# Optimization experiments

Hardware: AMD Instinct MI355X
Metric: run time of the kernel (lower is better)

The kernel has to match this reference:

```python
import jax, jax.numpy as jnp
import numpy as np

B, N, D, P = 4, 512, 512, 128

def setup_inputs() -> dict:
    key = jax.random.key(0)
    ks = jax.random.split(key, 8)
    s = lambda fan_in: 1.0 / np.sqrt(fan_in)
    inp = {
        "input": jax.random.normal(ks[0], (B, N, D), dtype=jnp.float32),
        # bigram projections (weights stored [in, out]; torch Linear is [out, in])
        "Wl": jax.random.uniform(ks[1], (D, P), jnp.float32, -s(D), s(D)),
        "bl": jnp.zeros((P,), jnp.float32),  # zeroed in initialize_parameters
        "Wr": jax.random.uniform(ks[2], (D, P), jnp.float32, -s(D), s(D)),  # no bias
        "Wo": jax.random.uniform(ks[3], (P, 1), jnp.float32, -s(P), s(P)),
        "bo": jnp.zeros((1,), jnp.float32),
        # start builder MLP
        "Ws1": jax.random.uniform(ks[4], (D, P), jnp.float32, -s(D), s(D)),
        "bs1": jnp.zeros((P,), jnp.float32),
        "Ws2": jax.random.uniform(ks[5], (P, 1), jnp.float32, -s(P), s(P)),
        "bs2": jnp.zeros((1,), jnp.float32),
        # end builder MLP
        "We1": jax.random.uniform(ks[6], (D, P), jnp.float32, -s(D), s(D)),
        "be1": jnp.zeros((P,), jnp.float32),
        "We2": jax.random.uniform(ks[7], (P, 1), jnp.float32, -s(P), s(P)),
        "be2": jnp.zeros((1,), jnp.float32),
    }
    return inp


def reference(input, Wl, bl, Wr, Wo, bo, Ws1, bs1, Ws2, bs2, We1, be1, We2, be2):
    # start / end unigram scores: [B, N, 1]
    start = jnp.maximum(input @ Ws1 + bs1, 0.0) @ Ws2 + bs2
    end = jnp.maximum(input @ We1 + be1, 0.0) @ We2 + be2
    # bigram scores
    left = input @ Wl + bl   # [B, N, P]
    right = input @ Wr       # [B, N, P]
    # left.unsqueeze(1) + right.unsqueeze(2) -> [B, N, N, P]
    proj = left[:, None, :, :] + right[:, :, None, :]
    bigram = jnp.maximum(proj, 0.0) @ Wo + bo  # [B, N, N, 1]
    return (bigram, start, end)
```

## Files before the change

kernel.cpp:

```cpp
#include <hip/hip_runtime.h>

typedef unsigned short ushort_t;
using f32x4  = __attribute__((ext_vector_type(4))) float;
using bf16x8 = __attribute__((ext_vector_type(8))) short;
using u16x8  = __attribute__((ext_vector_type(8))) unsigned short;
using h2v    = __attribute__((ext_vector_type(2))) _Float16;

constexpr int Bc = 4;
constexpr int Nc = 512;
constexpr int Dc = 512;
constexpr int Pc = 128;
constexpr int ROWS = Bc * Nc;

__device__ inline unsigned short f2bf(float f) {
    unsigned u = __builtin_bit_cast(unsigned, f);
    unsigned r = u + 0x7fffu + ((u >> 16) & 1u);
    return (unsigned short)(r >> 16);
}

__device__ inline void gload_lds16(const void* g, void* l) {
    __builtin_amdgcn_global_load_lds(
        (const __attribute__((address_space(1))) unsigned int*)g,
        (__attribute__((address_space(3))) unsigned int*)l, 16, 0, 0);
}

__device__ inline unsigned packh2(float a, float b) {
    unsigned short lo = __builtin_bit_cast(unsigned short, (_Float16)a);
    unsigned short hi = __builtin_bit_cast(unsigned short, (_Float16)b);
    return (unsigned)lo | ((unsigned)hi << 16);
}

__global__ __launch_bounds__(256) void convert_kernel(
    const float* __restrict__ input,
    const float* __restrict__ Wl,  const float* __restrict__ Wr,
    const float* __restrict__ Ws1, const float* __restrict__ We1,
    ushort_t* __restrict__ inBF2, ushort_t* __restrict__ WcatT2)
{
    const int bx = blockIdx.x, t = threadIdx.x;
    __shared__ float T[64][68];

    if (bx < 256) {
        const int mt = bx >> 3, ks = bx & 7;
        const int c = t & 7, r0 = t >> 3;
        const float* src = input + (size_t)(mt * 64) * Dc + ks * 64;
        ushort_t* dstc = inBF2 + ((size_t)(mt * 8 + ks) * 8 + c) * 512;
        #pragma unroll
        for (int h = 0; h < 2; ++h) {
            const int r = r0 + h * 32;
            const float* s = src + (size_t)r * Dc + c * 8;
            float4 v0 = *(const float4*)s;
            float4 v1 = *(const float4*)(s + 4);
            u16x8 o;
            o[0] = f2bf(v0.x); o[1] = f2bf(v0.y); o[2] = f2bf(v0.z); o[3] = f2bf(v0.w);
            o[4] = f2bf(v1.x); o[5] = f2bf(v1.y); o[6] = f2bf(v1.z); o[7] = f2bf(v1.w);
            *(u16x8*)(dstc + r * 8) = o;
        }
    } else {
        const int idx = bx - 256;
        const int nt = idx >> 3, ks = idx & 7;
        const int mi = nt >> 1, cm0 = (nt & 1) * 64;
        const float* Wm = (mi == 0) ? Wl : (mi == 1) ? Wr : (mi == 2) ? Ws1 : We1;

        const int kk_ = t >> 4, cc = (t & 15) << 2;
        #pragma unroll
        for (int u = 0; u < 4; ++u)
            *(float4*)&T[kk_ + 16 * u][cc] =
                *(const float4*)&Wm[(size_t)(ks * 64 + kk_ + 16 * u) * Pc + cm0 + cc];
        __syncthreads();

        const int col = t & 63, c2 = t >> 6;
        #pragma unroll
        for (int h = 0; h < 2; ++h) {
            const int kc = c2 + h * 4;
            u16x8 o;
            #pragma unroll
            for (int i = 0; i < 8; ++i) o[i] = f2bf(T[kc * 8 + i][col]);
            *(u16x8*)(WcatT2 + ((size_t)(nt * 8 + ks) * 8 + kc) * 512 + col * 8) = o;
        }
    }
}

__global__ __launch_bounds__(256) void mfma_proj3(
    const ushort_t* __restrict__ inBF2, const ushort_t* __restrict__ WcatT2,
    const float* __restrict__ bl,
    const float* __restrict__ bs1, const float* __restrict__ Ws2,
    const float* __restrict__ be1, const float* __restrict__ We2,
    ushort_t* __restrict__ leftH, ushort_t* __restrict__ rightH,
    float* __restrict__ parts)
{
    const int mt2 = blockIdx.x, ny = blockIdx.y;
    const int row0 = mt2 * 32;
    const int t = threadIdx.x, w = t >> 6, l = t & 63;
    const int wm = w & 1, wn = w >> 1;
    const int fr = l & 15, fg = l >> 4;

    __shared__ ushort_t As[2][2048];
    __shared__ ushort_t Bs[2][4096];
    __shared__ float red[64];

    const ushort_t* Atile = inBF2 + (size_t)(mt2 >> 1) * 8 * 4096;
    const int h32 = (mt2 & 1) * 32;
    const ushort_t* Bbase = WcatT2 + (size_t)ny * 8 * 4096;

    f32x4 acc0 = {0.f, 0.f, 0.f, 0.f}, acc1 = {0.f, 0.f, 0.f, 0.f};

#define PSTAGE(BI, KS)                                                         \
    {                                                                          \
        const ushort_t* ga = Atile + (KS) * 4096;                              \
        const ushort_t* gb = Bbase + (KS) * 4096;                              \
        gload_lds16(ga + (2 * w + (l >> 5)) * 512 + (h32 + (l & 31)) * 8,      \
                    &As[BI][w * 512]);                                         \
        gload_lds16(gb + w * 512 + l * 8, &Bs[BI][w * 512]);                   \
        gload_lds16(gb + (w + 4) * 512 + l * 8, &Bs[BI][(w + 4) * 512]);       \
    }

    PSTAGE(0, 0);
    __syncthreads();

    for (int ks = 0; ks < 8; ++ks) {
        const int bi = ks & 1;
        if (ks < 7) PSTAGE(bi ^ 1, ks + 1);
        #pragma unroll
        for (int kk = 0; kk < 2; ++kk) {
            const int kc = kk * 4 + fg;
            bf16x8 a  = *(const bf16x8*)&As[bi][kc * 256 + (wm * 16 + fr) * 8];
            bf16x8 b0 = *(const bf16x8*)&Bs[bi][kc * 512 + (wn * 32 + fr) * 8];
            bf16x8 b1 = *(const bf16x8*)&Bs[bi][kc * 512 + (wn * 32 + 16 + fr) * 8];
            acc0 = __builtin_amdgcn_mfma_f32_16x16x32_bf16(a, b0, acc0, 0, 0, 0);
            acc1 = __builtin_amdgcn_mfma_f32_16x16x32_bf16(a, b1, acc1, 0, 0, 0);
        }
        __syncthreads();
    }
#undef PSTAGE

    const int fq4 = fg << 2;
    if (ny < 4) {
        ushort_t* outp = (ny < 2) ? leftH : rightH;
        const int cb = (ny & 1) * 64 + wn * 32;
        #pragma unroll
        for (int n = 0; n < 2; ++n) {
            const int col = cb + n * 16 + fr;
            const float bv = (ny < 2) ? bl[col] : 0.f;
            const f32x4 av = n ? acc1 : acc0;
            #pragma unroll
            for (int q = 0; q < 4; ++q) {
                float v = av[q] + bv;
                outp[(size_t)(row0 + wm * 16 + fq4 + q) * Pc + col] =
                    __builtin_bit_cast(ushort_t, (_Float16)v);
            }
        }
    } else {
        const int pi = ny - 4;
        const float* b1 = (ny < 6) ? bs1 : be1;
        const float* W2 = (ny < 6) ? Ws2 : We2;
        const int pb = (pi & 1) * 64;
        #pragma unroll
        for (int q = 0; q < 4; ++q) {
            const int cp0 = pb + wn * 32 + fr;
            const int cp1 = pb + wn * 32 + 16 + fr;
            float v = fmaxf(acc0[q] + b1[cp0], 0.f) * W2[cp0]
                    + fmaxf(acc1[q] + b1[cp1], 0.f) * W2[cp1];
            v += __shfl_xor(v, 1);
            v += __shfl_xor(v, 2);
            v += __shfl_xor(v, 4);
            v += __shfl_xor(v, 8);
            if (fr == 0) red[wn * 32 + wm * 16 + fq4 + q] = v;
        }
        __syncthreads();
        if (t < 32) parts[pi * ROWS + row0 + t] = red[t] + red[32 + t];
    }
}

__global__ __launch_bounds__(256) void bigram_kernel(
    const ushort_t* __restrict__ leftH, const ushort_t* __restrict__ rightH,
    const float* __restrict__ Wo,   const float* __restrict__ bo,
    const float* __restrict__ parts,
    const float* __restrict__ bs2,  const float* __restrict__ be2,
    float* __restrict__ out, float* __restrict__ start_out,
    float* __restrict__ end_out)
{
    const int jt = blockIdx.x, it = blockIdx.y, b = blockIdx.z;
    const int t  = threadIdx.x;

    if (jt == 16) {
        const int base = (b * 8 + it) * 64;
        if (t < 64) {
            const int r = base + t;
            start_out[r] = parts[r] + parts[ROWS + r] + bs2[0];
        } else if (t < 128) {
            const int r = base + t - 64;
            end_out[r] = parts[2 * ROWS + r] + parts[3 * ROWS + r] + be2[0];
        }
        return;
    }

    __shared__ unsigned Lh[32][68];
    __shared__ unsigned Rh[64][68];
    __shared__ unsigned woh[64];

    const ushort_t* lp = leftH  + (size_t)(b * Nc + jt * 32) * Pc;
    const ushort_t* rp = rightH + (size_t)(b * Nc + it * 64) * Pc;

    #pragma unroll
    for (int u = 0; u < 2; ++u) {
        int f = t + u * 256, r = f >> 4, c = f & 15;
        *(float4*)&Lh[r][c * 4] = *(const float4*)(lp + (size_t)r * Pc + c * 8);
    }
    #pragma unroll
    for (int u = 0; u < 4; ++u) {
        int f = t + u * 256, r = f >> 4, c = f & 15;
        *(float4*)&Rh[r][c * 4] = *(const float4*)(rp + (size_t)r * Pc + c * 8);
    }
    if (t < 64) woh[t] = packh2(Wo[2 * t], Wo[2 * t + 1]);
    __syncthreads();

    const int jl = t & 15;
    const int il = t >> 4;

    float acc[4][2] = {};
    const h2v hz = {(_Float16)0.f, (_Float16)0.f};

#define DOTH(COMP)                                                       \
    {                                                                    \
        const unsigned wu = w4.COMP;                                     \
        h2v lv[2], rv[4];                                                \
        lv[0] = __builtin_bit_cast(h2v, l4[0].COMP);                     \
        lv[1] = __builtin_bit_cast(h2v, l4[1].COMP);                     \
        rv[0] = __builtin_bit_cast(h2v, r4[0].COMP);                     \
        rv[1] = __builtin_bit_cast(h2v, r4[1].COMP);                     \
        rv[2] = __builtin_bit_cast(h2v, r4[2].COMP);                     \
        rv[3] = __builtin_bit_cast(h2v, r4[3].COMP);                     \
        _Pragma("unroll") for (int ii = 0; ii < 4; ++ii)                 \
        _Pragma("unroll") for (int jj = 0; jj < 2; ++jj) {               \
            h2v sum = lv[jj] + rv[ii];                                   \
            sum = __builtin_elementwise_max(sum, hz);                    \
            unsigned su = __builtin_bit_cast(unsigned, sum);             \
            asm("v_dot2_f32_f16 %0, %1, %2, %0"                          \
                : "+v"(acc[ii][jj]) : "v"(su), "v"(wu));                 \
        }                                                                \
    }

    #pragma unroll 4
    for (int s4 = 0; s4 < 16; ++s4) {
        uint4 w4 = *(const uint4*)&woh[4 * s4];
        uint4 l4[2], r4[4];
        #pragma unroll
        for (int jj = 0; jj < 2; ++jj) l4[jj] = *(const uint4*)&Lh[jl + 16 * jj][4 * s4];
        #pragma unroll
        for (int ii = 0; ii < 4; ++ii) r4[ii] = *(const uint4*)&Rh[il + 16 * ii][4 * s4];
        DOTH(x) DOTH(y) DOTH(z) DOTH(w)
    }
#undef DOTH

    const float bias = bo[0];
    #pragma unroll
    for (int ii = 0; ii < 4; ++ii) {
        #pragma unroll
        for (int jj = 0; jj < 2; ++jj) {
            const int gi = it * 64 + il + 16 * ii;
            const int gj = jt * 32 + jl + 16 * jj;
            out[((size_t)b * Nc + gi) * Nc + gj] = acc[ii][jj] + bias;
        }
    }
}

extern "C" void kernel_launch(void* const* d_in, const int* in_sizes, int n_in,
                              void* d_out, int out_size, void* d_ws, size_t ws_size,
                              hipStream_t stream) {
    const float* input = (const float*)d_in[0];
    const float* Wl  = (const float*)d_in[1];
    const float* bl  = (const float*)d_in[2];
    const float* Wr  = (const float*)d_in[3];
    const float* Wo  = (const float*)d_in[4];
    const float* bo  = (const float*)d_in[5];
    const float* Ws1 = (const float*)d_in[6];
    const float* bs1 = (const float*)d_in[7];
    const float* Ws2 = (const float*)d_in[8];
    const float* bs2 = (const float*)d_in[9];
    const float* We1 = (const float*)d_in[10];
    const float* be1 = (const float*)d_in[11];
    const float* We2 = (const float*)d_in[12];
    const float* be2 = (const float*)d_in[13];

    float* out    = (float*)d_out;
    float* bigram = out;
    float* start  = out + (size_t)Bc * Nc * Nc;
    float* end    = start + (size_t)Bc * Nc;

    ushort_t* leftH  = (ushort_t*)d_ws;
    ushort_t* rightH = leftH + (size_t)ROWS * Pc;
    float* parts     = (float*)(rightH + (size_t)ROWS * Pc);
    ushort_t* inBF2  = (ushort_t*)(parts + 4 * ROWS);
    ushort_t* WcatT2 = inBF2 + (size_t)ROWS * Dc;

    convert_kernel<<<320, 256, 0, stream>>>(input, Wl, Wr, Ws1, We1, inBF2, WcatT2);

    mfma_proj3<<<dim3(64, 8), 256, 0, stream>>>(
        inBF2, WcatT2, bl, bs1, Ws2, be1, We2, leftH, rightH, parts);

    bigram_kernel<<<dim3(17, 8, 4), 256, 0, stream>>>(
        leftH, rightH, Wo, bo, parts, bs2, be2, bigram, start, end);
}
```

Before: 31.43 us.

## Fuse input bf16 conversion into projection GEMM A-tile loading

```diff
diff --git a/kernel.cpp b/kernel.cpp
--- a/kernel.cpp
+++ b/kernel.cpp
@@ -30,58 +30,38 @@
     return (unsigned)lo | ((unsigned)hi << 16);
 }
 
-__global__ __launch_bounds__(256) void convert_kernel(
-    const float* __restrict__ input,
+__global__ __launch_bounds__(256) void wconv_kernel(
     const float* __restrict__ Wl,  const float* __restrict__ Wr,
     const float* __restrict__ Ws1, const float* __restrict__ We1,
-    ushort_t* __restrict__ inBF2, ushort_t* __restrict__ WcatT2)
+    ushort_t* __restrict__ WcatT2)
 {
     const int bx = blockIdx.x, t = threadIdx.x;
     __shared__ float T[64][68];
 
-    if (bx < 256) {
-        const int mt = bx >> 3, ks = bx & 7;
-        const int c = t & 7, r0 = t >> 3;
-        const float* src = input + (size_t)(mt * 64) * Dc + ks * 64;
-        ushort_t* dstc = inBF2 + ((size_t)(mt * 8 + ks) * 8 + c) * 512;
-        #pragma unroll
-        for (int h = 0; h < 2; ++h) {
-            const int r = r0 + h * 32;
-            const float* s = src + (size_t)r * Dc + c * 8;
-            float4 v0 = *(const float4*)s;
-            float4 v1 = *(const float4*)(s + 4);
-            u16x8 o;
-            o[0] = f2bf(v0.x); o[1] = f2bf(v0.y); o[2] = f2bf(v0.z); o[3] = f2bf(v0.w);
-            o[4] = f2bf(v1.x); o[5] = f2bf(v1.y); o[6] = f2bf(v1.z); o[7] = f2bf(v1.w);
-            *(u16x8*)(dstc + r * 8) = o;
-        }
-    } else {
-        const int idx = bx - 256;
-        const int nt = idx >> 3, ks = idx & 7;
-        const int mi = nt >> 1, cm0 = (nt & 1) * 64;
-        const float* Wm = (mi == 0) ? Wl : (mi == 1) ? Wr : (mi == 2) ? Ws1 : We1;
-
-        const int kk_ = t >> 4, cc = (t & 15) << 2;
-        #pragma unroll
-        for (int u = 0; u < 4; ++u)
-            *(float4*)&T[kk_ + 16 * u][cc] =
-                *(const float4*)&Wm[(size_t)(ks * 64 + kk_ + 16 * u) * Pc + cm0 + cc];
-        __syncthreads();
-
-        const int col = t & 63, c2 = t >> 6;
-        #pragma unroll
-        for (int h = 0; h < 2; ++h) {
-            const int kc = c2 + h * 4;
-            u16x8 o;
-            #pragma unroll
-            for (int i = 0; i < 8; ++i) o[i] = f2bf(T[kc * 8 + i][col]);
-            *(u16x8*)(WcatT2 + ((size_t)(nt * 8 + ks) * 8 + kc) * 512 + col * 8) = o;
-        }
-    }
-}
-
-__global__ __launch_bounds__(256) void mfma_proj3(
-    const ushort_t* __restrict__ inBF2, const ushort_t* __restrict__ WcatT2,
+    const int nt = bx >> 3, ks = bx & 7;
+    const int mi = nt >> 1, cm0 = (nt & 1) * 64;
+    const float* Wm = (mi == 0) ? Wl : (mi == 1) ? Wr : (mi == 2) ? Ws1 : We1;
+
+    const int kk_ = t >> 4, cc = (t & 15) << 2;
+    #pragma unroll
+    for (int u = 0; u < 4; ++u)
+        *(float4*)&T[kk_ + 16 * u][cc] =
+            *(const float4*)&Wm[(size_t)(ks * 64 + kk_ + 16 * u) * Pc + cm0 + cc];
+    __syncthreads();
+
+    const int col = t & 63, c2 = t >> 6;
+    #pragma unroll
+    for (int h = 0; h < 2; ++h) {
+        const int kc = c2 + h * 4;
+        u16x8 o;
+        #pragma unroll
+        for (int i = 0; i < 8; ++i) o[i] = f2bf(T[kc * 8 + i][col]);
+        *(u16x8*)(WcatT2 + ((size_t)(nt * 8 + ks) * 8 + kc) * 512 + col * 8) = o;
+    }
+}
+
+__global__ __launch_bounds__(256) void mfma_proj4(
+    const float* __restrict__ input, const ushort_t* __restrict__ WcatT2,
     const float* __restrict__ bl,
     const float* __restrict__ bs1, const float* __restrict__ Ws2,
     const float* __restrict__ be1, const float* __restrict__ We2,
@@ -98,40 +78,78 @@
     __shared__ ushort_t Bs[2][4096];
     __shared__ float red[64];
 
-    const ushort_t* Atile = inBF2 + (size_t)(mt2 >> 1) * 8 * 4096;
-    const int h32 = (mt2 & 1) * 32;
     const ushort_t* Bbase = WcatT2 + (size_t)ny * 8 * 4096;
 
+    const int sr = t >> 3, skc = t & 7;
+    const float* Ain = input + (size_t)(row0 + sr) * Dc + skc * 8;
+    ushort_t* Ad0 = &As[0][skc * 256 + sr * 8];
+    ushort_t* Ad1 = &As[1][skc * 256 + sr * 8];
+
     f32x4 acc0 = {0.f, 0.f, 0.f, 0.f}, acc1 = {0.f, 0.f, 0.f, 0.f};
 
-#define PSTAGE(BI, KS)                                                         \
-    {                                                                          \
-        const ushort_t* ga = Atile + (KS) * 4096;                              \
-        const ushort_t* gb = Bbase + (KS) * 4096;                              \
-        gload_lds16(ga + (2 * w + (l >> 5)) * 512 + (h32 + (l & 31)) * 8,      \
-                    &As[BI][w * 512]);                                         \
-        gload_lds16(gb + w * 512 + l * 8, &Bs[BI][w * 512]);                   \
-        gload_lds16(gb + (w + 4) * 512 + l * 8, &Bs[BI][(w + 4) * 512]);       \
-    }
-
-    PSTAGE(0, 0);
+    float4 aE0, aE1, aO0, aO1;
+
+#define ALOAD(P0, P1, KS)                                     \
+    {                                                         \
+        const float* s_ = Ain + (KS) * 64;                    \
+        P0 = *(const float4*)s_;                              \
+        P1 = *(const float4*)(s_ + 4);                        \
+    }
+
+#define AWRITE(DST, P0, P1)                                   \
+    {                                                         \
+        u16x8 o_;                                             \
+        o_[0] = f2bf(P0.x); o_[1] = f2bf(P0.y);               \
+        o_[2] = f2bf(P0.z); o_[3] = f2bf(P0.w);               \
+        o_[4] = f2bf(P1.x); o_[5] = f2bf(P1.y);               \
+        o_[6] = f2bf(P1.z); o_[7] = f2bf(P1.w);               \
+        *(u16x8*)(DST) = o_;                                  \
+    }
+
+#define BSTAGE(BI, KS)                                                   \
+    {                                                                    \
+        const ushort_t* gb = Bbase + (KS) * 4096;                        \
+        gload_lds16(gb + w * 512 + l * 8, &Bs[BI][w * 512]);             \
+        gload_lds16(gb + (w + 4) * 512 + l * 8, &Bs[BI][(w + 4) * 512]); \
+    }
+
+#define COMPUTE(BI)                                                           \
+    {                                                                         \
+        _Pragma("unroll") for (int kk = 0; kk < 2; ++kk) {                    \
+            const int kc = kk * 4 + fg;                                       \
+            bf16x8 a  = *(const bf16x8*)&As[BI][kc * 256 + (wm * 16 + fr) * 8];       \
+            bf16x8 b0 = *(const bf16x8*)&Bs[BI][kc * 512 + (wn * 32 + fr) * 8];       \
+            bf16x8 b1 = *(const bf16x8*)&Bs[BI][kc * 512 + (wn * 32 + 16 + fr) * 8];  \
+            acc0 = __builtin_amdgcn_mfma_f32_16x16x32_bf16(a, b0, acc0, 0, 0, 0);     \
+            acc1 = __builtin_amdgcn_mfma_f32_16x16x32_bf16(a, b1, acc1, 0, 0, 0);     \
+        }                                                                     \
+    }
+
+    ALOAD(aE0, aE1, 0);
+    BSTAGE(0, 0);
+    AWRITE(Ad0, aE0, aE1);
+    ALOAD(aO0, aO1, 1);
     __syncthreads();
 
-    for (int ks = 0; ks < 8; ++ks) {
-        const int bi = ks & 1;
-        if (ks < 7) PSTAGE(bi ^ 1, ks + 1);
-        #pragma unroll
-        for (int kk = 0; kk < 2; ++kk) {
-            const int kc = kk * 4 + fg;
-            bf16x8 a  = *(const bf16x8*)&As[bi][kc * 256 + (wm * 16 + fr) * 8];
-            bf16x8 b0 = *(const bf16x8*)&Bs[bi][kc * 512 + (wn * 32 + fr) * 8];
-            bf16x8 b1 = *(const bf16x8*)&Bs[bi][kc * 512 + (wn * 32 + 16 + fr) * 8];
-            acc0 = __builtin_amdgcn_mfma_f32_16x16x32_bf16(a, b0, acc0, 0, 0, 0);
-            acc1 = __builtin_amdgcn_mfma_f32_16x16x32_bf16(a, b1, acc1, 0, 0, 0);
-        }
+    #pragma unroll
+    for (int ks2 = 0; ks2 < 8; ks2 += 2) {
+        BSTAGE(1, ks2 + 1);
+        if (ks2 + 2 < 8) ALOAD(aE0, aE1, ks2 + 2);
+        COMPUTE(0);
+        AWRITE(Ad1, aO0, aO1);
         __syncthreads();
-    }
-#undef PSTAGE
+        if (ks2 + 2 < 8) {
+            BSTAGE(0, ks2 + 2);
+            if (ks2 + 3 < 8) ALOAD(aO0, aO1, ks2 + 3);
+        }
+        COMPUTE(1);
+        if (ks2 + 2 < 8) AWRITE(Ad0, aE0, aE1);
+        __syncthreads();
+    }
+#undef ALOAD
+#undef AWRITE
+#undef BSTAGE
+#undef COMPUTE
 
     const int fq4 = fg << 2;
     if (ny < 4) {
@@ -290,13 +308,12 @@
     ushort_t* leftH  = (ushort_t*)d_ws;
     ushort_t* rightH = leftH + (size_t)ROWS * Pc;
     float* parts     = (float*)(rightH + (size_t)ROWS * Pc);
-    ushort_t* inBF2  = (ushort_t*)(parts + 4 * ROWS);
-    ushort_t* WcatT2 = inBF2 + (size_t)ROWS * Dc;
-
-    convert_kernel<<<320, 256, 0, stream>>>(input, Wl, Wr, Ws1, We1, inBF2, WcatT2);
-
-    mfma_proj3<<<dim3(64, 8), 256, 0, stream>>>(
-        inBF2, WcatT2, bl, bs1, Ws2, be1, We2, leftH, rightH, parts);
+    ushort_t* WcatT2 = (ushort_t*)(parts + 4 * ROWS);
+
+    wconv_kernel<<<64, 256, 0, stream>>>(Wl, Wr, Ws1, We1, WcatT2);
+
+    mfma_proj4<<<dim3(64, 8), 256, 0, stream>>>(
+        input, WcatT2, bl, bs1, Ws2, be1, We2, leftH, rightH, parts);
 
     bigram_kernel<<<dim3(17, 8, 4), 256, 0, stream>>>(
         leftH, rightH, Wo, bo, parts, bs2, be2, bigram, start, end);
```

Result: no change. 31.37 us (-0.2%).
